# Kernel optimization log

Measured on AMD Instinct MI355X. Metric: run time of the kernel, lower is better.

The kernel has to match this reference:

```python
import jax, jax.numpy as jnp
import numpy as np

DIM = 2048
NUM_EXPERTS = 64
NUM_TOKENS = 32768
CAPACITY_FACTOR = 1.0
EPSILON = 1e-6


def setup_inputs() -> dict:
    key = jax.random.key(0)
    k1, k2 = jax.random.split(key)
    x = jax.random.normal(k1, (NUM_TOKENS, DIM), dtype=jnp.float32)
    # nn.Linear(dim, num_experts): weight init ~ U(-1/sqrt(dim), 1/sqrt(dim))
    bound = 1.0 / np.sqrt(DIM)
    w_gate = jax.random.uniform(k2, (DIM, NUM_EXPERTS), dtype=jnp.float32,
                                minval=-bound, maxval=bound)
    b_gate = jnp.zeros((NUM_EXPERTS,), dtype=jnp.float32)
    return {"x": x, "w_gate": w_gate, "b_gate": b_gate}


def reference(x, w_gate, b_gate):
    # gate_scores = softmax(x @ W + b), shape [N, E]
    logits = jnp.einsum("nd,de->ne", x, w_gate) + b_gate
    gate_scores = jax.nn.softmax(logits, axis=-1)

    capacity = int(CAPACITY_FACTOR * x.shape[0])  # static

    # top-1 mask via argmax (equivalent to topk(1) + scatter of ones)
    top1 = jnp.argmax(gate_scores, axis=-1)                      # [N]
    mask = jax.nn.one_hot(top1, gate_scores.shape[-1],
                          dtype=gate_scores.dtype)               # [N, E]
    masked = gate_scores * mask

    # column-wise normalization, scaled by capacity
    denom = masked.sum(axis=0, keepdims=True) + EPSILON          # [1, E]
    return masked / denom * capacity
```

## Files before the change

kernel.cpp:

```cpp
#include <hip/hip_runtime.h>
#include <hip/hip_bf16.h>

#define DIM   2048
#define NEXP  64
#define NTOK  32768
#define KC    32
#define NC    64
#define TB    128
#define NBLK  (NTOK / TB)
#define NSLOT 5
#define BB    12288
#define WFOFF 1024

typedef __attribute__((ext_vector_type(8))) short bf16x8;
typedef __attribute__((ext_vector_type(4))) float f32x4;

typedef __attribute__((address_space(1))) const void gvoid_t;
typedef __attribute__((address_space(3))) void lvoid_t;
#define GLDS16(g, l) __builtin_amdgcn_global_load_lds((gvoid_t*)(g), (lvoid_t*)(l), 16, 0, 0)

__device__ __forceinline__ float rne_split(float v, short& h) {
    __hip_bfloat16 hb = __float2bfloat16(v);
    h = __builtin_bit_cast(short, hb);
    return __bfloat162float(hb);
}

__device__ __forceinline__ void split8(const float4& a, const float4& b,
                                       bf16x8& H, bf16x8& M, bf16x8& L) {
    const float vs[8] = {a.x, a.y, a.z, a.w, b.x, b.y, b.z, b.w};
#pragma unroll
    for (int j = 0; j < 8; ++j) {
        short h, m, l;
        const float fh = rne_split(vs[j], h);
        const float e1 = vs[j] - fh;
        const float fm = rne_split(e1, m);
        const float e2 = e1 - fm;
        rne_split(e2, l);
        H[j] = h; M[j] = m; L[j] = l;
    }
}

__global__ __launch_bounds__(256)
void wsplit_kernel(const float* __restrict__ w, bf16x8* __restrict__ wf,
                   float* __restrict__ denom) {
    if (blockIdx.x == 0 && threadIdx.x < NEXP) denom[threadIdx.x] = 0.0f;
    const int tid  = blockIdx.x * 256 + threadIdx.x;
    const int lane = tid & 63;
    const int ni   = (tid >> 6) & 3;
    const int ks   = tid >> 8;
    const int n    = ni * 16 + (lane & 15);
    const int k0   = ks * KC + (lane >> 4) * 8;
    bf16x8 H, M, L;
#pragma unroll
    for (int j = 0; j < 8; ++j) {
        const float v = w[(size_t)(k0 + j) * NEXP + n];
        short h, m, l;
        const float fh = rne_split(v, h);
        const float e1 = v - fh;
        const float fm = rne_split(e1, m);
        rne_split(e1 - fm, l);
        H[j] = h; M[j] = m; L[j] = l;
    }
    wf[((size_t)(ks * 3 + 0) * 4 + ni) * 64 + lane] = H;
    wf[((size_t)(ks * 3 + 1) * 4 + ni) * 64 + lane] = M;
    wf[((size_t)(ks * 3 + 2) * 4 + ni) * 64 + lane] = L;
}

__global__ __launch_bounds__(256, 1)
void gate_kernel(const float* __restrict__ x, const bf16x8* __restrict__ wf,
                 const float* __restrict__ b, float* __restrict__ out,
                 float* __restrict__ denom)
{
    __shared__ __align__(16) char slab[NSLOT * BB];
    __shared__ float dlds[NEXP];

    const int tid  = threadIdx.x;
    const int lane = tid & 63;
    const int l15  = lane & 15;
    const int l4   = lane >> 4;
    const int wv   = tid >> 6;
    const int tok0 = blockIdx.x * TB;

    if (tid < NEXP) dlds[tid] = 0.0f;

    float bias[4];
#pragma unroll
    for (int ni = 0; ni < 4; ++ni) bias[ni] = b[ni * 16 + l15];

    const float* xr0 = x + (size_t)(tok0 + wv * 32 + l15) * DIM + l4 * 8;
    const float* xr1 = xr0 + (size_t)16 * DIM;

#define LOADX(X, c) {                                                  \
    X[0] = *(const float4*)(xr0 + (size_t)(c) * KC);                   \
    X[1] = *(const float4*)(xr0 + (size_t)(c) * KC + 4);               \
    X[2] = *(const float4*)(xr1 + (size_t)(c) * KC);                   \
    X[3] = *(const float4*)(xr1 + (size_t)(c) * KC + 4); }

#define STAGE(slot, c) {                                               \
    const char* _src = (const char*)wf + (size_t)(c) * BB + tid * 16;  \
    char* _dst = slab + (size_t)(slot) * BB + tid * 16;                \
    GLDS16(_src, _dst);                                                \
    GLDS16(_src + 4096, _dst + 4096);                                  \
    GLDS16(_src + 8192, _dst + 8192); }

    f32x4 acc[2][4];
#pragma unroll
    for (int mi = 0; mi < 2; ++mi)
#pragma unroll
        for (int ni = 0; ni < 4; ++ni) acc[mi][ni] = (f32x4){0.f, 0.f, 0.f, 0.f};

    float4 xa[4], xb[4];
    STAGE(0, 0)
    __builtin_amdgcn_sched_barrier(0);
    STAGE(1, 1)
    __builtin_amdgcn_sched_barrier(0);
    LOADX(xa, 0)
    __builtin_amdgcn_sched_barrier(0);
    STAGE(2, 2)
    __builtin_amdgcn_sched_barrier(0);
    LOADX(xb, 1)
    __builtin_amdgcn_sched_barrier(0);
    STAGE(3, 3)
    __builtin_amdgcn_sched_barrier(0);

#define ITER(c, scomp, sstage, XC) {                                   \
    asm volatile("s_waitcnt vmcnt(10)" ::: "memory");                  \
    __builtin_amdgcn_s_barrier();                                      \
    __builtin_amdgcn_sched_barrier(0);                                 \
    const bf16x8* _bl = (const bf16x8*)(slab + (size_t)(scomp) * BB);  \
    bf16x8 Bf[12];                                                     \
    _Pragma("unroll")                                                  \
    for (int _f = 0; _f < 12; ++_f) Bf[_f] = _bl[_f * 64 + lane];      \
    __builtin_amdgcn_sched_barrier(0);                                 \
    bf16x8 Ah0, Am0, Al0, Ah1, Am1, Al1;                               \
    split8(XC[0], XC[1], Ah0, Am0, Al0);                               \
    split8(XC[2], XC[3], Ah1, Am1, Al1);                               \
    __builtin_amdgcn_sched_barrier(0);                                 \
    { const int _cx = ((c) + 2 < NC) ? (c) + 2 : NC - 1;               \
      LOADX(XC, _cx) }                                                 \
    __builtin_amdgcn_sched_barrier(0);                                 \
    { const int _cs = ((c) + 4 < NC) ? (c) + 4 : NC - 1;               \
      STAGE(sstage, _cs) }                                             \
    __builtin_amdgcn_sched_barrier(0);                                 \
    _Pragma("unroll")                                                  \
    for (int _ni = 0; _ni < 4; ++_ni) {                                \
        f32x4 _a0 = acc[0][_ni], _a1 = acc[1][_ni];                    \
        _a0 = __builtin_amdgcn_mfma_f32_16x16x32_bf16(Ah0, Bf[_ni],     _a0, 0, 0, 0); \
        _a1 = __builtin_amdgcn_mfma_f32_16x16x32_bf16(Ah1, Bf[_ni],     _a1, 0, 0, 0); \
        _a0 = __builtin_amdgcn_mfma_f32_16x16x32_bf16(Ah0, Bf[4 + _ni], _a0, 0, 0, 0); \
        _a1 = __builtin_amdgcn_mfma_f32_16x16x32_bf16(Ah1, Bf[4 + _ni], _a1, 0, 0, 0); \
        _a0 = __builtin_amdgcn_mfma_f32_16x16x32_bf16(Am0, Bf[_ni],     _a0, 0, 0, 0); \
        _a1 = __builtin_amdgcn_mfma_f32_16x16x32_bf16(Am1, Bf[_ni],     _a1, 0, 0, 0); \
        _a0 = __builtin_amdgcn_mfma_f32_16x16x32_bf16(Ah0, Bf[8 + _ni], _a0, 0, 0, 0); \
        _a1 = __builtin_amdgcn_mfma_f32_16x16x32_bf16(Ah1, Bf[8 + _ni], _a1, 0, 0, 0); \
        _a0 = __builtin_amdgcn_mfma_f32_16x16x32_bf16(Am0, Bf[4 + _ni], _a0, 0, 0, 0); \
        _a1 = __builtin_amdgcn_mfma_f32_16x16x32_bf16(Am1, Bf[4 + _ni], _a1, 0, 0, 0); \
        _a0 = __builtin_amdgcn_mfma_f32_16x16x32_bf16(Al0, Bf[_ni],     _a0, 0, 0, 0); \
        _a1 = __builtin_amdgcn_mfma_f32_16x16x32_bf16(Al1, Bf[_ni],     _a1, 0, 0, 0); \
        acc[0][_ni] = _a0; acc[1][_ni] = _a1;                          \
    } }

    int scomp = 0, sstage = 4;
#pragma unroll 1
    for (int c = 0; c < NC; c += 2) {
        ITER(c, scomp, sstage, xa)
        if (++scomp == NSLOT) scomp = 0;
        if (++sstage == NSLOT) sstage = 0;
        ITER(c + 1, scomp, sstage, xb)
        if (++scomp == NSLOT) scomp = 0;
        if (++sstage == NSLOT) sstage = 0;
    }

    asm volatile("s_waitcnt vmcnt(0)" ::: "memory");
    __syncthreads();

#pragma unroll
    for (int mi = 0; mi < 2; ++mi)
#pragma unroll
        for (int r = 0; r < 4; ++r) {
            const float v0 = acc[mi][0][r] + bias[0];
            const float v1 = acc[mi][1][r] + bias[1];
            const float v2 = acc[mi][2][r] + bias[2];
            const float v3 = acc[mi][3][r] + bias[3];

            float lm = v0; int le = l15;
            if (v1 > lm) { lm = v1; le = l15 + 16; }
            if (v2 > lm) { lm = v2; le = l15 + 32; }
            if (v3 > lm) { lm = v3; le = l15 + 48; }
#pragma unroll
            for (int off = 1; off < 16; off <<= 1) {
                const float om = __shfl_xor(lm, off);
                const int   oe = __shfl_xor(le, off);
                if (om > lm || (om == lm && oe < le)) { lm = om; le = oe; }
            }
            float s = __expf(v0 - lm) + __expf(v1 - lm) +
                      __expf(v2 - lm) + __expf(v3 - lm);
#pragma unroll
            for (int off = 1; off < 16; off <<= 1) s += __shfl_xor(s, off);
            const float g = 1.0f / s;

            const int t = tok0 + wv * 32 + mi * 16 + 4 * l4 + r;
            float* orow = out + (size_t)t * NEXP + l15;
            orow[0]  = (le == l15     ) ? g : 0.0f;
            orow[16] = (le == l15 + 16) ? g : 0.0f;
            orow[32] = (le == l15 + 32) ? g : 0.0f;
            orow[48] = (le == l15 + 48) ? g : 0.0f;
            if (l15 == 0) atomicAdd(&dlds[le], g);
        }

    __syncthreads();
    if (tid < NEXP) atomicAdd(&denom[tid], dlds[tid]);
}

__global__ __launch_bounds__(256)
void scale_kernel(float* __restrict__ out, const float* __restrict__ denom)
{
    __shared__ float sc[NEXP];
    if (threadIdx.x < NEXP)
        sc[threadIdx.x] = (float)NTOK / (denom[threadIdx.x] + 1e-6f);
    __syncthreads();

    const size_t i = (size_t)blockIdx.x * blockDim.x + threadIdx.x;
    float4 v = ((const float4*)out)[i];
    const int e0 = (int)((i * 4) & (NEXP - 1));
    v.x *= sc[e0]; v.y *= sc[e0 + 1]; v.z *= sc[e0 + 2]; v.w *= sc[e0 + 3];
    ((float4*)out)[i] = v;
}

extern "C" void kernel_launch(void* const* d_in, const int* in_sizes, int n_in,
                              void* d_out, int out_size, void* d_ws, size_t ws_size,
                              hipStream_t stream) {
    const float* x = (const float*)d_in[0];
    const float* w = (const float*)d_in[1];
    const float* b = (const float*)d_in[2];
    float*  out   = (float*)d_out;
    float*  denom = (float*)d_ws;
    bf16x8* wf    = (bf16x8*)((char*)d_ws + WFOFF);

    wsplit_kernel<<<64, 256, 0, stream>>>(w, wf, denom);
    gate_kernel<<<NBLK, 256, 0, stream>>>(x, wf, b, out, denom);
    scale_kernel<<<(NTOK * NEXP / 4) / 256, 256, 0, stream>>>(out, denom);
}
```

Baseline: 87.61 us.

## Halve tokens per block to 64 and run two blocks per CU

Each block now handles 64 tokens instead of 128. Every wave computes one 16-row MFMA tile instead of two, so the x register buffers and accumulators shrink, and launch bounds allow two blocks per CU. The aim is to raise occupancy and latency hiding for the x streaming while the grid doubles to 512 blocks. In exchange, the split-bf16 weight fragments are staged into LDS twice as often in total, since each block reuses them over fewer tokens. The 60 KB LDS slab per block must also fit twice per CU.

```diff
diff --git a/kernel.cpp b/kernel.cpp
--- a/kernel.cpp
+++ b/kernel.cpp
@@ -6,7 +6,7 @@
 #define NTOK  32768
 #define KC    32
 #define NC    64
-#define TB    128
+#define TB    64
 #define NBLK  (NTOK / TB)
 #define NSLOT 5
 #define BB    12288
@@ -66,7 +66,7 @@
     wf[((size_t)(ks * 3 + 2) * 4 + ni) * 64 + lane] = L;
 }
 
-__global__ __launch_bounds__(256, 1)
+__global__ __launch_bounds__(256, 2)
 void gate_kernel(const float* __restrict__ x, const bf16x8* __restrict__ wf,
                  const float* __restrict__ b, float* __restrict__ out,
                  float* __restrict__ denom)
@@ -87,14 +87,11 @@
 #pragma unroll
     for (int ni = 0; ni < 4; ++ni) bias[ni] = b[ni * 16 + l15];
 
-    const float* xr0 = x + (size_t)(tok0 + wv * 32 + l15) * DIM + l4 * 8;
-    const float* xr1 = xr0 + (size_t)16 * DIM;
+    const float* xr0 = x + (size_t)(tok0 + wv * 16 + l15) * DIM + l4 * 8;
 
 #define LOADX(X, c) {                                                  \
     X[0] = *(const float4*)(xr0 + (size_t)(c) * KC);                   \
-    X[1] = *(const float4*)(xr0 + (size_t)(c) * KC + 4);               \
-    X[2] = *(const float4*)(xr1 + (size_t)(c) * KC);                   \
-    X[3] = *(const float4*)(xr1 + (size_t)(c) * KC + 4); }
+    X[1] = *(const float4*)(xr0 + (size_t)(c) * KC + 4); }
 
 #define STAGE(slot, c) {                                               \
     const char* _src = (const char*)wf + (size_t)(c) * BB + tid * 16;  \
@@ -103,13 +100,11 @@
     GLDS16(_src + 4096, _dst + 4096);                                  \
     GLDS16(_src + 8192, _dst + 8192); }
 
-    f32x4 acc[2][4];
-#pragma unroll
-    for (int mi = 0; mi < 2; ++mi)
-#pragma unroll
-        for (int ni = 0; ni < 4; ++ni) acc[mi][ni] = (f32x4){0.f, 0.f, 0.f, 0.f};
-
-    float4 xa[4], xb[4];
+    f32x4 acc[4];
+#pragma unroll
+    for (int ni = 0; ni < 4; ++ni) acc[ni] = (f32x4){0.f, 0.f, 0.f, 0.f};
+
+    float4 xa[2], xb[2];
     STAGE(0, 0)
     __builtin_amdgcn_sched_barrier(0);
     STAGE(1, 1)
@@ -124,7 +119,7 @@
     __builtin_amdgcn_sched_barrier(0);
 
 #define ITER(c, scomp, sstage, XC) {                                   \
-    asm volatile("s_waitcnt vmcnt(10)" ::: "memory");                  \
+    asm volatile("s_waitcnt vmcnt(8)" ::: "memory");                   \
     __builtin_amdgcn_s_barrier();                                      \
     __builtin_amdgcn_sched_barrier(0);                                 \
     const bf16x8* _bl = (const bf16x8*)(slab + (size_t)(scomp) * BB);  \
@@ -132,9 +127,8 @@
     _Pragma("unroll")                                                  \
     for (int _f = 0; _f < 12; ++_f) Bf[_f] = _bl[_f * 64 + lane];      \
     __builtin_amdgcn_sched_barrier(0);                                 \
-    bf16x8 Ah0, Am0, Al0, Ah1, Am1, Al1;                               \
-    split8(XC[0], XC[1], Ah0, Am0, Al0);                               \
-    split8(XC[2], XC[3], Ah1, Am1, Al1);                               \
+    bf16x8 Ah, Am, Al;                                                 \
+    split8(XC[0], XC[1], Ah, Am, Al);                                  \
     __builtin_amdgcn_sched_barrier(0);                                 \
     { const int _cx = ((c) + 2 < NC) ? (c) + 2 : NC - 1;               \
       LOADX(XC, _cx) }                                                 \
@@ -144,20 +138,14 @@
     __builtin_amdgcn_sched_barrier(0);                                 \
     _Pragma("unroll")                                                  \
     for (int _ni = 0; _ni < 4; ++_ni) {                                \
-        f32x4 _a0 = acc[0][_ni], _a1 = acc[1][_ni];                    \
-        _a0 = __builtin_amdgcn_mfma_f32_16x16x32_bf16(Ah0, Bf[_ni],     _a0, 0, 0, 0); \
-        _a1 = __builtin_amdgcn_mfma_f32_16x16x32_bf16(Ah1, Bf[_ni],     _a1, 0, 0, 0); \
-        _a0 = __builtin_amdgcn_mfma_f32_16x16x32_bf16(Ah0, Bf[4 + _ni], _a0, 0, 0, 0); \
-        _a1 = __builtin_amdgcn_mfma_f32_16x16x32_bf16(Ah1, Bf[4 + _ni], _a1, 0, 0, 0); \
-        _a0 = __builtin_amdgcn_mfma_f32_16x16x32_bf16(Am0, Bf[_ni],     _a0, 0, 0, 0); \
-        _a1 = __builtin_amdgcn_mfma_f32_16x16x32_bf16(Am1, Bf[_ni],     _a1, 0, 0, 0); \
-        _a0 = __builtin_amdgcn_mfma_f32_16x16x32_bf16(Ah0, Bf[8 + _ni], _a0, 0, 0, 0); \
-        _a1 = __builtin_amdgcn_mfma_f32_16x16x32_bf16(Ah1, Bf[8 + _ni], _a1, 0, 0, 0); \
-        _a0 = __builtin_amdgcn_mfma_f32_16x16x32_bf16(Am0, Bf[4 + _ni], _a0, 0, 0, 0); \
-        _a1 = __builtin_amdgcn_mfma_f32_16x16x32_bf16(Am1, Bf[4 + _ni], _a1, 0, 0, 0); \
-        _a0 = __builtin_amdgcn_mfma_f32_16x16x32_bf16(Al0, Bf[_ni],     _a0, 0, 0, 0); \
-        _a1 = __builtin_amdgcn_mfma_f32_16x16x32_bf16(Al1, Bf[_ni],     _a1, 0, 0, 0); \
-        acc[0][_ni] = _a0; acc[1][_ni] = _a1;                          \
+        f32x4 _a = acc[_ni];                                           \
+        _a = __builtin_amdgcn_mfma_f32_16x16x32_bf16(Ah, Bf[_ni],     _a, 0, 0, 0); \
+        _a = __builtin_amdgcn_mfma_f32_16x16x32_bf16(Ah, Bf[4 + _ni], _a, 0, 0, 0); \
+        _a = __builtin_amdgcn_mfma_f32_16x16x32_bf16(Am, Bf[_ni],     _a, 0, 0, 0); \
+        _a = __builtin_amdgcn_mfma_f32_16x16x32_bf16(Ah, Bf[8 + _ni], _a, 0, 0, 0); \
+        _a = __builtin_amdgcn_mfma_f32_16x16x32_bf16(Am, Bf[4 + _ni], _a, 0, 0, 0); \
+        _a = __builtin_amdgcn_mfma_f32_16x16x32_bf16(Al, Bf[_ni],     _a, 0, 0, 0); \
+        acc[_ni] = _a;                                                 \
     } }
 
     int scomp = 0, sstage = 4;
@@ -175,38 +163,36 @@
     __syncthreads();
 
 #pragma unroll
-    for (int mi = 0; mi < 2; ++mi)
-#pragma unroll
-        for (int r = 0; r < 4; ++r) {
-            const float v0 = acc[mi][0][r] + bias[0];
-            const float v1 = acc[mi][1][r] + bias[1];
-            const float v2 = acc[mi][2][r] + bias[2];
-            const float v3 = acc[mi][3][r] + bias[3];
-
-            float lm = v0; int le = l15;
-            if (v1 > lm) { lm = v1; le = l15 + 16; }
-            if (v2 > lm) { lm = v2; le = l15 + 32; }
-            if (v3 > lm) { lm = v3; le = l15 + 48; }
-#pragma unroll
-            for (int off = 1; off < 16; off <<= 1) {
-                const float om = __shfl_xor(lm, off);
-                const int   oe = __shfl_xor(le, off);
-                if (om > lm || (om == lm && oe < le)) { lm = om; le = oe; }
-            }
-            float s = __expf(v0 - lm) + __expf(v1 - lm) +
-                      __expf(v2 - lm) + __expf(v3 - lm);
-#pragma unroll
-            for (int off = 1; off < 16; off <<= 1) s += __shfl_xor(s, off);
-            const float g = 1.0f / s;
-
-            const int t = tok0 + wv * 32 + mi * 16 + 4 * l4 + r;
-            float* orow = out + (size_t)t * NEXP + l15;
-            orow[0]  = (le == l15     ) ? g : 0.0f;
-            orow[16] = (le == l15 + 16) ? g : 0.0f;
-            orow[32] = (le == l15 + 32) ? g : 0.0f;
-            orow[48] = (le == l15 + 48) ? g : 0.0f;
-            if (l15 == 0) atomicAdd(&dlds[le], g);
+    for (int r = 0; r < 4; ++r) {
+        const float v0 = acc[0][r] + bias[0];
+        const float v1 = acc[1][r] + bias[1];
+        const float v2 = acc[2][r] + bias[2];
+        const float v3 = acc[3][r] + bias[3];
+
+        float lm = v0; int le = l15;
+        if (v1 > lm) { lm = v1; le = l15 + 16; }
+        if (v2 > lm) { lm = v2; le = l15 + 32; }
+        if (v3 > lm) { lm = v3; le = l15 + 48; }
+#pragma unroll
+        for (int off = 1; off < 16; off <<= 1) {
+            const float om = __shfl_xor(lm, off);
+            const int   oe = __shfl_xor(le, off);
+            if (om > lm || (om == lm && oe < le)) { lm = om; le = oe; }
         }
+        float s = __expf(v0 - lm) + __expf(v1 - lm) +
+                  __expf(v2 - lm) + __expf(v3 - lm);
+#pragma unroll
+        for (int off = 1; off < 16; off <<= 1) s += __shfl_xor(s, off);
+        const float g = 1.0f / s;
+
+        const int t = tok0 + wv * 16 + 4 * l4 + r;
+        float* orow = out + (size_t)t * NEXP + l15;
+        orow[0]  = (le == l15     ) ? g : 0.0f;
+        orow[16] = (le == l15 + 16) ? g : 0.0f;
+        orow[32] = (le == l15 + 32) ? g : 0.0f;
+        orow[48] = (le == l15 + 48) ? g : 0.0f;
+        if (l15 == 0) atomicAdd(&dlds[le], g);
+    }
 
     __syncthreads();
     if (tid < NEXP) atomicAdd(&denom[tid], dlds[tid]);
```

Result: faster. 80.40 us (median of 2 runs) (-8.2%).
